# Kernel optimization log

Hardware: AMD Instinct MI355X
Metric: run time of the kernel (lower is better)

Reference implementation:

```python
import jax, jax.numpy as jnp
import numpy as np

HEAD_DIM = 64

def setup_inputs() -> dict:
    key = jax.random.key(0)
    kq, kk, kv = jax.random.split(key, 3)
    shape = (2, 4096, 8, HEAD_DIM)  # [B, S, H, D]
    q = jax.random.normal(kq, shape, dtype=jnp.float32)
    k = jax.random.normal(kk, shape, dtype=jnp.float32)
    v = jax.random.normal(kv, shape, dtype=jnp.float32)
    return {"q": q, "k": k, "v": v}

def reference(q, k, v):
    # Single-process path of SimpleRingAttention: standard softmax attention.
    # q,k,v: [B, S, H, D]; scores computed per head.
    scale = 1.0 / jnp.sqrt(jnp.asarray(HEAD_DIM, dtype=q.dtype))
    scores = jnp.einsum('bqhd,bkhd->bhqk', q, k) * scale  # [B,H,S,S]
    attn = jax.nn.softmax(scores, axis=-1)
    out = jnp.einsum('bhqk,bkhd->bqhd', attn, v)  # back to [B,S,H,D]
    return out
```

## Files before the change

kernel.cpp:

```cpp
#include <hip/hip_runtime.h>
#include <hip/hip_bf16.h>

#define B_ 2
#define S_ 4096
#define H_ 8
#define D_ 64
#define BQ 128
#define BK 64

#define GLOBAL_AS __attribute__((address_space(1)))
#define LDS_AS    __attribute__((address_space(3)))

typedef short bf16x8 __attribute__((ext_vector_type(8)));
typedef short bf16x4 __attribute__((ext_vector_type(4)));
typedef float f32x4  __attribute__((ext_vector_type(4)));

#define QSCALE 0.18033688011112043f

__device__ __forceinline__ short f2bf(float f) {
    __bf16 h = (__bf16)f;
    return __builtin_bit_cast(short, h);
}

__device__ __forceinline__ bf16x8 pack8(float4 f0, float4 f1) {
    bf16x8 r;
    r[0]=f2bf(f0.x); r[1]=f2bf(f0.y); r[2]=f2bf(f0.z); r[3]=f2bf(f0.w);
    r[4]=f2bf(f1.x); r[5]=f2bf(f1.y); r[6]=f2bf(f1.z); r[7]=f2bf(f1.w);
    return r;
}

__device__ __forceinline__ bf16x8 pack8s(float4 f0, float4 f1, float s) {
    bf16x8 r;
    r[0]=f2bf(f0.x*s); r[1]=f2bf(f0.y*s); r[2]=f2bf(f0.z*s); r[3]=f2bf(f0.w*s);
    r[4]=f2bf(f1.x*s); r[5]=f2bf(f1.y*s); r[6]=f2bf(f1.z*s); r[7]=f2bf(f1.w*s);
    return r;
}

__global__ __launch_bounds__(256) void cast_kv_kernel(
    const float* __restrict__ kin, const float* __restrict__ vin,
    unsigned short* __restrict__ kb, unsigned short* __restrict__ vtb)
{
    __shared__ float Lf[64][72];
    const int role = blockIdx.z & 1;
    const int b    = blockIdx.z >> 1;
    const int h    = blockIdx.y;
    const int s0   = blockIdx.x * 64;
    const int t    = threadIdx.x;

    if (role == 0) {
        int r = t >> 2, fq = t & 3;
        const float4* gp = (const float4*)(kin + (((size_t)(b*S_ + s0 + r)*H_ + h)*D_ + fq*16));
        bf16x8 o0 = pack8(gp[0], gp[1]);
        bf16x8 o1 = pack8(gp[2], gp[3]);
        unsigned short* ob = kb + ((size_t)(b*H_ + h)*S_ + s0 + r)*D_ + fq*16;
        *(bf16x8*)ob       = o0;
        *(bf16x8*)(ob + 8) = o1;
    } else {
        {
            int r  = t >> 2, fq = t & 3;
            const float4* gp = (const float4*)(vin + (((size_t)(b*S_ + s0 + r)*H_ + h)*D_ + fq*16));
            #pragma unroll
            for (int j = 0; j < 4; ++j)
                *(f32x4*)&Lf[r][fq*16 + 4*j] = (f32x4){gp[j].x, gp[j].y, gp[j].z, gp[j].w};
        }
        __syncthreads();
        {
            int d = t >> 2, sq = t & 3;
            bf16x8 o0, o1;
            #pragma unroll
            for (int j = 0; j < 8; ++j) o0[j] = f2bf(Lf[sq*16 + j][d]);
            #pragma unroll
            for (int j = 0; j < 8; ++j) o1[j] = f2bf(Lf[sq*16 + 8 + j][d]);
            unsigned short* ob = vtb + (((size_t)(b*H_ + h)*D_ + d)*S_ + s0 + sq*16);
            *(bf16x8*)(ob)     = o0;
            *(bf16x8*)(ob + 8) = o1;
        }
    }
}

template<bool SPLIT>
__global__ __launch_bounds__(256, 4) void fattn_kernel(
    const float* __restrict__ q, const unsigned short* __restrict__ kb,
    const unsigned short* __restrict__ vtb, float* __restrict__ out,
    float* __restrict__ Op, float* __restrict__ lw)
{
    __shared__ unsigned short Ks [BK][64];
    __shared__ unsigned short Vts[D_][64];
    __shared__ unsigned short Ps [BQ][64];

    const int tid  = threadIdx.x;
    const int wave = tid >> 6;
    const int lane = tid & 63;
    const int m16  = tid & 15;
    const int quad = (tid & 63) >> 4;
    const int h    = blockIdx.y;
    const int b    = SPLIT ? (blockIdx.z >> 1) : blockIdx.z;
    const int half = SPLIT ? (blockIdx.z & 1)  : 0;
    const int kt0  = half * 32;
    const int nkt  = SPLIT ? 32 : 64;
    const int q0   = blockIdx.x * BQ;
    const int bS   = b * S_;
    const int wq2  = wave * 32;
    const int r7   = m16 & 7;

    int ksoff[2][4];
    #pragma unroll
    for (int kh = 0; kh < 2; ++kh)
        #pragma unroll
        for (int t4 = 0; t4 < 4; ++t4)
            ksoff[kh][t4] = (t4*16 + m16)*64 + (((kh*4 + quad) ^ r7)*8);
    int proff[2][2];
    #pragma unroll
    for (int n = 0; n < 2; ++n)
        #pragma unroll
        for (int kh = 0; kh < 2; ++kh)
            proff[n][kh] = (wq2 + n*16 + m16)*64 + (((kh*4 + quad) ^ r7)*8);
    int pwoff[2][4];
    #pragma unroll
    for (int n = 0; n < 2; ++n)
        #pragma unroll
        for (int mt = 0; mt < 4; ++mt)
            pwoff[n][mt] = (wq2 + n*16 + m16)*64
                         + (((2*mt + (quad>>1)) ^ r7)*8) + (quad&1)*4;

    const int srow = (lane >> 3);
    const int c8g  = (lane & 7) ^ srow;
    const int wqs  = wave * 16;
    const unsigned short* ksg[2];
    const unsigned short* vtg[2];
    #pragma unroll
    for (int it = 0; it < 2; ++it) {
        int rk = wqs + it*8 + srow;
        ksg[it] = kb  + ((size_t)(b*H_ + h)*S_ + rk)*64 + c8g*8;
        vtg[it] = vtb + ((size_t)(b*H_ + h)*D_ + rk)*(size_t)S_ + c8g*8;
    }

    bf16x8 bq[2][2];
    #pragma unroll
    for (int n = 0; n < 2; ++n) {
        const int qrow = q0 + wq2 + n*16 + m16;
        const float* qp = q + ((size_t)(bS + qrow)*H_ + h)*D_;
        #pragma unroll
        for (int kh = 0; kh < 2; ++kh) {
            const float4* q4 = (const float4*)(qp + kh*32 + quad*8);
            bq[n][kh] = pack8s(q4[0], q4[1], QSCALE);
        }
    }

    const short ONE = 0x3F80;
    bf16x8 ones = { ONE,ONE,ONE,ONE,ONE,ONE,ONE,ONE };

    f32x4 oacc[2][4];
    f32x4 lacc[2];
    #pragma unroll
    for (int n = 0; n < 2; ++n) {
        lacc[n] = (f32x4){0.f,0.f,0.f,0.f};
        #pragma unroll
        for (int dt = 0; dt < 4; ++dt) oacc[n][dt] = (f32x4){0.f,0.f,0.f,0.f};
    }

    for (int i = 0; i < nkt; ++i) {
        const int kt = kt0 + i;
        __syncthreads();

        #pragma unroll
        for (int it = 0; it < 2; ++it) {
            __builtin_amdgcn_global_load_lds(
                (const GLOBAL_AS void*)(ksg[it] + (size_t)kt*BK*64),
                (LDS_AS void*)&Ks[wqs + it*8][0], 16, 0, 0);
            __builtin_amdgcn_global_load_lds(
                (const GLOBAL_AS void*)(vtg[it] + (size_t)kt*BK),
                (LDS_AS void*)&Vts[wqs + it*8][0], 16, 0, 0);
        }
        __syncthreads();

        #pragma unroll
        for (int mt = 0; mt < 4; ++mt) {
            f32x4 s0 = (f32x4){0.f,0.f,0.f,0.f};
            f32x4 s1 = (f32x4){0.f,0.f,0.f,0.f};
            #pragma unroll
            for (int kh = 0; kh < 2; ++kh) {
                bf16x8 aK = *(const bf16x8*)&Ks[0][ksoff[kh][mt]];
                s0 = __builtin_amdgcn_mfma_f32_16x16x32_bf16(aK, bq[0][kh], s0, 0,0,0);
                s1 = __builtin_amdgcn_mfma_f32_16x16x32_bf16(aK, bq[1][kh], s1, 0,0,0);
            }
            bf16x4 p0, p1;
            #pragma unroll
            for (int r = 0; r < 4; ++r) {
                p0[r] = f2bf(__builtin_exp2f(s0[r]));
                p1[r] = f2bf(__builtin_exp2f(s1[r]));
            }
            *(bf16x4*)&Ps[0][pwoff[0][mt]] = p0;
            *(bf16x4*)&Ps[0][pwoff[1][mt]] = p1;
        }

        #pragma unroll
        for (int kh = 0; kh < 2; ++kh) {
            bf16x8 bp0 = *(const bf16x8*)&Ps[0][proff[0][kh]];
            bf16x8 bp1 = *(const bf16x8*)&Ps[0][proff[1][kh]];
            lacc[0] = __builtin_amdgcn_mfma_f32_16x16x32_bf16(ones, bp0, lacc[0], 0,0,0);
            lacc[1] = __builtin_amdgcn_mfma_f32_16x16x32_bf16(ones, bp1, lacc[1], 0,0,0);
            #pragma unroll
            for (int dt = 0; dt < 4; ++dt) {
                bf16x8 aV = *(const bf16x8*)&Vts[0][ksoff[kh][dt]];
                oacc[0][dt] = __builtin_amdgcn_mfma_f32_16x16x32_bf16(aV, bp0, oacc[0][dt], 0,0,0);
                oacc[1][dt] = __builtin_amdgcn_mfma_f32_16x16x32_bf16(aV, bp1, oacc[1][dt], 0,0,0);
            }
        }
    }

    #pragma unroll
    for (int n = 0; n < 2; ++n) {
        const int orow = q0 + wq2 + n*16 + m16;
        if constexpr (SPLIT) {
            float* ob = Op + (size_t)half*((size_t)B_*S_*H_*D_)
                           + ((size_t)(bS + orow)*H_ + h)*D_;
            #pragma unroll
            for (int dt = 0; dt < 4; ++dt) {
                float4 o4 = { oacc[n][dt][0], oacc[n][dt][1],
                              oacc[n][dt][2], oacc[n][dt][3] };
                *(float4*)(ob + dt*16 + quad*4) = o4;
            }
            if (quad == 0)
                lw[(size_t)half*((size_t)B_*S_*H_) + (size_t)(bS + orow)*H_ + h] = lacc[n][0];
        } else {
            const float linv = 1.0f / lacc[n][0];
            float* ob = out + ((size_t)(bS + orow)*H_ + h)*D_;
            #pragma unroll
            for (int dt = 0; dt < 4; ++dt) {
                float4 o4 = { oacc[n][dt][0]*linv, oacc[n][dt][1]*linv,
                              oacc[n][dt][2]*linv, oacc[n][dt][3]*linv };
                *(float4*)(ob + dt*16 + quad*4) = o4;
            }
        }
    }
}

__global__ __launch_bounds__(256) void combine_kernel(
    const float* __restrict__ Op, const float* __restrict__ lw,
    float* __restrict__ out)
{
    const size_t NR = (size_t)B_*S_*H_;
    const size_t NO = NR * D_;
    const int t = threadIdx.x;
    size_t r  = (size_t)blockIdx.x * 16 + (t >> 4);
    int   c4  = t & 15;
    const float4* p0 = (const float4*)(Op + r*D_) + c4;
    const float4* p1 = (const float4*)(Op + NO + r*D_) + c4;
    float linv = 1.0f / (lw[r] + lw[NR + r]);
    float4 a = *p0, b = *p1;
    float4 o = { (a.x+b.x)*linv, (a.y+b.y)*linv, (a.z+b.z)*linv, (a.w+b.w)*linv };
    *((float4*)(out + r*D_) + c4) = o;
}

#define FBQ 64
#define LDK 72
__global__ __launch_bounds__(256, 4) void fattn_fb(
    const float* __restrict__ q, const float* __restrict__ k,
    const float* __restrict__ v, float* __restrict__ out)
{
    __shared__ unsigned short Ks [BK][LDK];
    __shared__ unsigned short Vts[D_][LDK];
    __shared__ unsigned short Ps [FBQ][LDK];
    const int tid  = threadIdx.x;
    const int wave = tid >> 6;
    const int m16  = tid & 15;
    const int quad = (tid & 63) >> 4;
    const int h    = blockIdx.y;
    const int b    = blockIdx.z;
    const int q0   = blockIdx.x * FBQ;
    const int bS   = b * S_;
    const int wq   = wave * 16;
    bf16x8 bq[2];
    {
        const int qrow = q0 + wq + m16;
        const float* qb = q + ((size_t)(bS + qrow)*H_ + h)*D_;
        #pragma unroll
        for (int kh = 0; kh < 2; ++kh) {
            const float4* qp = (const float4*)(qb + kh*32 + quad*8);
            bq[kh] = pack8s(qp[0], qp[1], QSCALE);
        }
    }
    const short ONE = 0x3F80;
    bf16x8 ones = { ONE,ONE,ONE,ONE,ONE,ONE,ONE,ONE };
    f32x4 oacc[4];
    f32x4 lacc = (f32x4){0.f,0.f,0.f,0.f};
    #pragma unroll
    for (int dt = 0; dt < 4; ++dt) oacc[dt] = (f32x4){0.f,0.f,0.f,0.f};
    const int vd  = tid & 63;
    const int vkg = tid >> 6;
    for (int kt = 0; kt < S_/BK; ++kt) {
        const int k0 = kt * BK;
        __syncthreads();
        #pragma unroll
        for (int i = 0; i < 2; ++i) {
            int chunk = tid + i*256;
            int row = chunk >> 3, c8 = chunk & 7;
            const float4* gp = (const float4*)(k + ((size_t)(bS + k0 + row)*H_ + h)*D_ + c8*8);
            *(bf16x8*)&Ks[row][c8*8] = pack8(gp[0], gp[1]);
        }
        {
            const float* vb = v + ((size_t)(bS + k0 + vkg*16)*H_ + h)*D_ + vd;
            bf16x8 t0, t1;
            #pragma unroll
            for (int i = 0; i < 8; ++i) t0[i] = f2bf(vb[(size_t)i * (H_*D_)]);
            #pragma unroll
            for (int i = 0; i < 8; ++i) t1[i] = f2bf(vb[(size_t)(i+8) * (H_*D_)]);
            *(bf16x8*)&Vts[vd][vkg*16]     = t0;
            *(bf16x8*)&Vts[vd][vkg*16 + 8] = t1;
        }
        __syncthreads();
        f32x4 sacc[4];
        #pragma unroll
        for (int mt = 0; mt < 4; ++mt) sacc[mt] = (f32x4){0.f,0.f,0.f,0.f};
        #pragma unroll
        for (int kh = 0; kh < 2; ++kh)
            #pragma unroll
            for (int mt = 0; mt < 4; ++mt) {
                bf16x8 aK = *(const bf16x8*)&Ks[mt*16 + m16][kh*32 + quad*8];
                sacc[mt] = __builtin_amdgcn_mfma_f32_16x16x32_bf16(aK, bq[kh], sacc[mt], 0,0,0);
            }
        #pragma unroll
        for (int mt = 0; mt < 4; ++mt) {
            bf16x4 pk;
            #pragma unroll
            for (int r = 0; r < 4; ++r)
                pk[r] = f2bf(__builtin_exp2f(sacc[mt][r]));
            *(bf16x4*)&Ps[wq + m16][mt*16 + quad*4] = pk;
        }
        #pragma unroll
        for (int kh = 0; kh < 2; ++kh) {
            bf16x8 bp = *(const bf16x8*)&Ps[wq + m16][kh*32 + quad*8];
            lacc = __builtin_amdgcn_mfma_f32_16x16x32_bf16(ones, bp, lacc, 0,0,0);
            #pragma unroll
            for (int dt = 0; dt < 4; ++dt) {
                bf16x8 aV = *(const bf16x8*)&Vts[dt*16 + m16][kh*32 + quad*8];
                oacc[dt] = __builtin_amdgcn_mfma_f32_16x16x32_bf16(aV, bp, oacc[dt], 0,0,0);
            }
        }
    }
    const float linv = 1.0f / lacc[0];
    const int orow = q0 + wq + m16;
    float* ob = out + ((size_t)(bS + orow)*H_ + h)*D_;
    #pragma unroll
    for (int dt = 0; dt < 4; ++dt) {
        float4 o4 = { oacc[dt][0]*linv, oacc[dt][1]*linv,
                      oacc[dt][2]*linv, oacc[dt][3]*linv };
        *(float4*)(ob + dt*16 + quad*4) = o4;
    }
}

extern "C" void kernel_launch(void* const* d_in, const int* in_sizes, int n_in,
                              void* d_out, int out_size, void* d_ws, size_t ws_size,
                              hipStream_t stream) {
    const float* q = (const float*)d_in[0];
    const float* k = (const float*)d_in[1];
    const float* v = (const float*)d_in[2];
    float* out = (float*)d_out;
    const size_t elems = (size_t)B_*H_*S_*D_;
    const size_t NR    = (size_t)B_*S_*H_;
    const size_t need_cast  = 2 * elems * sizeof(unsigned short);
    const size_t need_split = need_cast + 2*elems*sizeof(float) + 2*NR*sizeof(float);

    if (ws_size >= need_split) {
        unsigned short* kb  = (unsigned short*)d_ws;
        unsigned short* vtb = kb + elems;
        float* Op = (float*)(vtb + elems);
        float* lw = Op + 2*elems;
        cast_kv_kernel<<<dim3(S_/64, H_, B_*2), dim3(256), 0, stream>>>(k, v, kb, vtb);
        fattn_kernel<true><<<dim3(S_/BQ, H_, B_*2), dim3(256), 0, stream>>>(
            q, kb, vtb, out, Op, lw);
        combine_kernel<<<dim3((int)(NR/16)), dim3(256), 0, stream>>>(Op, lw, out);
    } else if (ws_size >= need_cast) {
        unsigned short* kb  = (unsigned short*)d_ws;
        unsigned short* vtb = kb + elems;
        cast_kv_kernel<<<dim3(S_/64, H_, B_*2), dim3(256), 0, stream>>>(k, v, kb, vtb);
        fattn_kernel<false><<<dim3(S_/BQ, H_, B_), dim3(256), 0, stream>>>(
            q, kb, vtb, out, nullptr, nullptr);
    } else {
        fattn_fb<<<dim3(S_/FBQ, H_, B_), dim3(256), 0, stream>>>(q, k, v, out);
    }
}
```

Before: 196.7 us.

## Switch attention to 32x32x16 MFMA with register-resident P via permlane swap

Replaces the 16x16x32 MFMA tiling with 32x32x16 MFMAs so each wave handles 32 query rows in one tile. The probability matrix P no longer goes through LDS: the exponentiated scores are packed to bf16 and rearranged into B-operand layout with v_permlane32_swap. The row sum is now accumulated with scalar adds plus one final shuffle instead of an MFMA against a ones vector. This removes the LDS round trip and the extra MFMAs for P and the row sum, at the cost of more register pressure from the 16-wide accumulators and a permlane instruction that only exists on newer CDNA parts.

```diff
diff --git a/kernel.cpp b/kernel.cpp
--- a/kernel.cpp
+++ b/kernel.cpp
@@ -14,6 +14,8 @@
 typedef short bf16x8 __attribute__((ext_vector_type(8)));
 typedef short bf16x4 __attribute__((ext_vector_type(4)));
 typedef float f32x4  __attribute__((ext_vector_type(4)));
+typedef float f32x16 __attribute__((ext_vector_type(16)));
+typedef unsigned int u32x4 __attribute__((ext_vector_type(4)));
 
 #define QSCALE 0.18033688011112043f
 
@@ -34,6 +36,16 @@
     r[0]=f2bf(f0.x*s); r[1]=f2bf(f0.y*s); r[2]=f2bf(f0.z*s); r[3]=f2bf(f0.w*s);
     r[4]=f2bf(f1.x*s); r[5]=f2bf(f1.y*s); r[6]=f2bf(f1.z*s); r[7]=f2bf(f1.w*s);
     return r;
+}
+
+__device__ __forceinline__ unsigned pkbf(float a, float b) {
+    unsigned ua = (unsigned)(unsigned short)__builtin_bit_cast(unsigned short, (__bf16)a);
+    unsigned ub = (unsigned)(unsigned short)__builtin_bit_cast(unsigned short, (__bf16)b);
+    return ua | (ub << 16);
+}
+
+__device__ __forceinline__ void perm32swap(unsigned &a, unsigned &b) {
+    asm("v_permlane32_swap_b32 %0, %1" : "+v"(a), "+v"(b));
 }
 
 __global__ __launch_bounds__(256) void cast_kv_kernel(
@@ -86,13 +98,12 @@
 {
     __shared__ unsigned short Ks [BK][64];
     __shared__ unsigned short Vts[D_][64];
-    __shared__ unsigned short Ps [BQ][64];
 
     const int tid  = threadIdx.x;
     const int wave = tid >> 6;
     const int lane = tid & 63;
-    const int m16  = tid & 15;
-    const int quad = (tid & 63) >> 4;
+    const int l31  = tid & 31;
+    const int hi   = lane >> 5;
     const int h    = blockIdx.y;
     const int b    = SPLIT ? (blockIdx.z >> 1) : blockIdx.z;
     const int half = SPLIT ? (blockIdx.z & 1)  : 0;
@@ -100,28 +111,14 @@
     const int nkt  = SPLIT ? 32 : 64;
     const int q0   = blockIdx.x * BQ;
     const int bS   = b * S_;
-    const int wq2  = wave * 32;
-    const int r7   = m16 & 7;
-
-    int ksoff[2][4];
-    #pragma unroll
-    for (int kh = 0; kh < 2; ++kh)
-        #pragma unroll
-        for (int t4 = 0; t4 < 4; ++t4)
-            ksoff[kh][t4] = (t4*16 + m16)*64 + (((kh*4 + quad) ^ r7)*8);
-    int proff[2][2];
-    #pragma unroll
-    for (int n = 0; n < 2; ++n)
-        #pragma unroll
-        for (int kh = 0; kh < 2; ++kh)
-            proff[n][kh] = (wq2 + n*16 + m16)*64 + (((kh*4 + quad) ^ r7)*8);
-    int pwoff[2][4];
-    #pragma unroll
-    for (int n = 0; n < 2; ++n)
-        #pragma unroll
-        for (int mt = 0; mt < 4; ++mt)
-            pwoff[n][mt] = (wq2 + n*16 + m16)*64
-                         + (((2*mt + (quad>>1)) ^ r7)*8) + (quad&1)*4;
+    const int wq   = wave * 32;
+
+    int aoff[2][4];
+    #pragma unroll
+    for (int t = 0; t < 2; ++t)
+        #pragma unroll
+        for (int kc = 0; kc < 4; ++kc)
+            aoff[t][kc] = (t*32 + l31)*64 + (((kc*2 + hi) ^ (l31 & 7))*8);
 
     const int srow = (lane >> 3);
     const int c8g  = (lane & 7) ^ srow;
@@ -135,34 +132,27 @@
         vtg[it] = vtb + ((size_t)(b*H_ + h)*D_ + rk)*(size_t)S_ + c8g*8;
     }
 
-    bf16x8 bq[2][2];
-    #pragma unroll
-    for (int n = 0; n < 2; ++n) {
-        const int qrow = q0 + wq2 + n*16 + m16;
+    bf16x8 bq[4];
+    {
+        const int qrow = q0 + wq + l31;
         const float* qp = q + ((size_t)(bS + qrow)*H_ + h)*D_;
         #pragma unroll
-        for (int kh = 0; kh < 2; ++kh) {
-            const float4* q4 = (const float4*)(qp + kh*32 + quad*8);
-            bq[n][kh] = pack8s(q4[0], q4[1], QSCALE);
-        }
-    }
-
-    const short ONE = 0x3F80;
-    bf16x8 ones = { ONE,ONE,ONE,ONE,ONE,ONE,ONE,ONE };
-
-    f32x4 oacc[2][4];
-    f32x4 lacc[2];
-    #pragma unroll
-    for (int n = 0; n < 2; ++n) {
-        lacc[n] = (f32x4){0.f,0.f,0.f,0.f};
-        #pragma unroll
-        for (int dt = 0; dt < 4; ++dt) oacc[n][dt] = (f32x4){0.f,0.f,0.f,0.f};
-    }
+        for (int kc = 0; kc < 4; ++kc) {
+            const float4* q4 = (const float4*)(qp + kc*16 + hi*8);
+            bq[kc] = pack8s(q4[0], q4[1], QSCALE);
+        }
+    }
+
+    f32x16 oacc[2];
+    #pragma unroll
+    for (int dt = 0; dt < 2; ++dt)
+        #pragma unroll
+        for (int r = 0; r < 16; ++r) oacc[dt][r] = 0.f;
+    float lp0 = 0.f, lp1 = 0.f;
 
     for (int i = 0; i < nkt; ++i) {
         const int kt = kt0 + i;
         __syncthreads();
-
         #pragma unroll
         for (int it = 0; it < 2; ++it) {
             __builtin_amdgcn_global_load_lds(
@@ -175,64 +165,70 @@
         __syncthreads();
 
         #pragma unroll
-        for (int mt = 0; mt < 4; ++mt) {
-            f32x4 s0 = (f32x4){0.f,0.f,0.f,0.f};
-            f32x4 s1 = (f32x4){0.f,0.f,0.f,0.f};
-            #pragma unroll
-            for (int kh = 0; kh < 2; ++kh) {
-                bf16x8 aK = *(const bf16x8*)&Ks[0][ksoff[kh][mt]];
-                s0 = __builtin_amdgcn_mfma_f32_16x16x32_bf16(aK, bq[0][kh], s0, 0,0,0);
-                s1 = __builtin_amdgcn_mfma_f32_16x16x32_bf16(aK, bq[1][kh], s1, 0,0,0);
-            }
-            bf16x4 p0, p1;
-            #pragma unroll
-            for (int r = 0; r < 4; ++r) {
-                p0[r] = f2bf(__builtin_exp2f(s0[r]));
-                p1[r] = f2bf(__builtin_exp2f(s1[r]));
-            }
-            *(bf16x4*)&Ps[0][pwoff[0][mt]] = p0;
-            *(bf16x4*)&Ps[0][pwoff[1][mt]] = p1;
-        }
-
-        #pragma unroll
-        for (int kh = 0; kh < 2; ++kh) {
-            bf16x8 bp0 = *(const bf16x8*)&Ps[0][proff[0][kh]];
-            bf16x8 bp1 = *(const bf16x8*)&Ps[0][proff[1][kh]];
-            lacc[0] = __builtin_amdgcn_mfma_f32_16x16x32_bf16(ones, bp0, lacc[0], 0,0,0);
-            lacc[1] = __builtin_amdgcn_mfma_f32_16x16x32_bf16(ones, bp1, lacc[1], 0,0,0);
-            #pragma unroll
-            for (int dt = 0; dt < 4; ++dt) {
-                bf16x8 aV = *(const bf16x8*)&Vts[0][ksoff[kh][dt]];
-                oacc[0][dt] = __builtin_amdgcn_mfma_f32_16x16x32_bf16(aV, bp0, oacc[0][dt], 0,0,0);
-                oacc[1][dt] = __builtin_amdgcn_mfma_f32_16x16x32_bf16(aV, bp1, oacc[1][dt], 0,0,0);
-            }
-        }
-    }
-
-    #pragma unroll
-    for (int n = 0; n < 2; ++n) {
-        const int orow = q0 + wq2 + n*16 + m16;
-        if constexpr (SPLIT) {
-            float* ob = Op + (size_t)half*((size_t)B_*S_*H_*D_)
-                           + ((size_t)(bS + orow)*H_ + h)*D_;
-            #pragma unroll
-            for (int dt = 0; dt < 4; ++dt) {
-                float4 o4 = { oacc[n][dt][0], oacc[n][dt][1],
-                              oacc[n][dt][2], oacc[n][dt][3] };
-                *(float4*)(ob + dt*16 + quad*4) = o4;
-            }
-            if (quad == 0)
-                lw[(size_t)half*((size_t)B_*S_*H_) + (size_t)(bS + orow)*H_ + h] = lacc[n][0];
-        } else {
-            const float linv = 1.0f / lacc[n][0];
-            float* ob = out + ((size_t)(bS + orow)*H_ + h)*D_;
-            #pragma unroll
-            for (int dt = 0; dt < 4; ++dt) {
-                float4 o4 = { oacc[n][dt][0]*linv, oacc[n][dt][1]*linv,
-                              oacc[n][dt][2]*linv, oacc[n][dt][3]*linv };
-                *(float4*)(ob + dt*16 + quad*4) = o4;
-            }
-        }
+        for (int mt = 0; mt < 2; ++mt) {
+            f32x16 s;
+            #pragma unroll
+            for (int r = 0; r < 16; ++r) s[r] = 0.f;
+            #pragma unroll
+            for (int kc = 0; kc < 4; ++kc) {
+                bf16x8 aK = *(const bf16x8*)&Ks[0][aoff[mt][kc]];
+                s = __builtin_amdgcn_mfma_f32_32x32x16_bf16(aK, bq[kc], s, 0,0,0);
+            }
+
+            unsigned pk_[8];
+            #pragma unroll
+            for (int r = 0; r < 8; ++r) {
+                float e0 = __builtin_exp2f(s[2*r]);
+                float e1 = __builtin_exp2f(s[2*r+1]);
+                lp0 += e0; lp1 += e1;
+                pk_[r] = pkbf(e0, e1);
+            }
+            perm32swap(pk_[0], pk_[2]);
+            perm32swap(pk_[1], pk_[3]);
+            perm32swap(pk_[4], pk_[6]);
+            perm32swap(pk_[5], pk_[7]);
+            u32x4 w0 = {pk_[0], pk_[1], pk_[2], pk_[3]};
+            u32x4 w1 = {pk_[4], pk_[5], pk_[6], pk_[7]};
+            bf16x8 bp0 = __builtin_bit_cast(bf16x8, w0);
+            bf16x8 bp1 = __builtin_bit_cast(bf16x8, w1);
+
+            #pragma unroll
+            for (int dt = 0; dt < 2; ++dt) {
+                bf16x8 aV0 = *(const bf16x8*)&Vts[0][aoff[dt][mt*2 + 0]];
+                oacc[dt] = __builtin_amdgcn_mfma_f32_32x32x16_bf16(aV0, bp0, oacc[dt], 0,0,0);
+                bf16x8 aV1 = *(const bf16x8*)&Vts[0][aoff[dt][mt*2 + 1]];
+                oacc[dt] = __builtin_amdgcn_mfma_f32_32x32x16_bf16(aV1, bp1, oacc[dt], 0,0,0);
+            }
+        }
+    }
+
+    float lt0 = lp0 + lp1;
+    float lt  = lt0 + __shfl_xor(lt0, 32);
+    const int orow = q0 + wq + l31;
+    if constexpr (SPLIT) {
+        float* ob = Op + (size_t)half*((size_t)B_*S_*H_*D_)
+                       + ((size_t)(bS + orow)*H_ + h)*D_;
+        #pragma unroll
+        for (int dt = 0; dt < 2; ++dt)
+            #pragma unroll
+            for (int rg = 0; rg < 4; ++rg) {
+                float4 o4 = { oacc[dt][rg*4+0], oacc[dt][rg*4+1],
+                              oacc[dt][rg*4+2], oacc[dt][rg*4+3] };
+                *(float4*)(ob + dt*32 + rg*8 + hi*4) = o4;
+            }
+        if (hi == 0)
+            lw[(size_t)half*((size_t)B_*S_*H_) + (size_t)(bS + orow)*H_ + h] = lt;
+    } else {
+        const float linv = 1.0f / lt;
+        float* ob = out + ((size_t)(bS + orow)*H_ + h)*D_;
+        #pragma unroll
+        for (int dt = 0; dt < 2; ++dt)
+            #pragma unroll
+            for (int rg = 0; rg < 4; ++rg) {
+                float4 o4 = { oacc[dt][rg*4+0]*linv, oacc[dt][rg*4+1]*linv,
+                              oacc[dt][rg*4+2]*linv, oacc[dt][rg*4+3]*linv };
+                *(float4*)(ob + dt*32 + rg*8 + hi*4) = o4;
+            }
     }
 }
 
```

Measured after the change: 209.3 us. 6.4% more time.
